# Performance work log

Measured on AMD Instinct MI355X. Metric: run time of the kernel, lower is better.

## Reference

```python
import jax, jax.numpy as jnp
import numpy as np

N, E, G = 100000, 1600000, 1000
F_IN, H, C = 16, 64, 2
EPS = 1e-5


def setup_inputs() -> dict:
    key = jax.random.key(0)
    ks = jax.random.split(key, 8)

    def lin(k, i, o):
        return (jax.random.normal(k, (i, o), jnp.float32) / np.float32(np.sqrt(i)))

    return {
        "x": jax.random.normal(ks[0], (N, F_IN), jnp.float32),
        "edge_index": jax.random.randint(ks[1], (2, E), 0, N),
        "batch": jnp.sort(jax.random.randint(ks[2], (N,), 0, G)),
        # GraphNorm params: weight=1, bias=0, mean_scale(alpha)=1 (PyG init)
        "gn0_w": jnp.ones(F_IN, jnp.float32), "gn0_b": jnp.zeros(F_IN, jnp.float32), "gn0_a": jnp.ones(F_IN, jnp.float32),
        "W1": lin(ks[3], F_IN, H), "b1": jnp.zeros(H, jnp.float32),
        "gn1_w": jnp.ones(H, jnp.float32), "gn1_b": jnp.zeros(H, jnp.float32), "gn1_a": jnp.ones(H, jnp.float32),
        "W2": lin(ks[4], H, H), "b2": jnp.zeros(H, jnp.float32),
        "gn2_w": jnp.ones(H, jnp.float32), "gn2_b": jnp.zeros(H, jnp.float32), "gn2_a": jnp.ones(H, jnp.float32),
        "W3": lin(ks[5], H, H), "b3": jnp.zeros(H, jnp.float32),
        "Wd": lin(ks[6], H, H), "bd": jnp.zeros(H, jnp.float32),
        "Wo": lin(ks[7], H, C), "bo": jnp.zeros(C, jnp.float32),
    }


def _graph_norm(x, batch, w, b, a):
    counts = jnp.maximum(jax.ops.segment_sum(jnp.ones(x.shape[0], x.dtype), batch, G), 1.0)[:, None]
    mean = jax.ops.segment_sum(x, batch, G) / counts          # [G, F]
    out = x - a * mean[batch]
    var = jax.ops.segment_sum(out * out, batch, G) / counts   # [G, F]
    return w * (out * jax.lax.rsqrt(var + EPS)[batch]) + b


def _gcn_conv(x, W, b, src, dst):
    # PyG GCNConv: D^{-1/2}(A+I)D^{-1/2} X W + b, deg includes self-loop
    h = x @ W                                                  # [N, out]
    deg = jax.ops.segment_sum(jnp.ones(src.shape[0], x.dtype), dst, N) + 1.0
    dinv = jax.lax.rsqrt(deg)
    msg = h[src] * (dinv[src] * dinv[dst])[:, None]            # [E, out]
    agg = jax.ops.segment_sum(msg, dst, N) + h / deg[:, None]  # self-loop term: 1/deg
    return agg + b


def reference(x, edge_index, batch, gn0_w, gn0_b, gn0_a, W1, b1,
              gn1_w, gn1_b, gn1_a, W2, b2, gn2_w, gn2_b, gn2_a,
              W3, b3, Wd, bd, Wo, bo):
    src, dst = edge_index[0], edge_index[1]
    x = _graph_norm(x, batch, gn0_w, gn0_b, gn0_a)
    x = jax.nn.relu(_gcn_conv(x, W1, b1, src, dst))
    x = _graph_norm(x, batch, gn1_w, gn1_b, gn1_a)
    x = jax.nn.relu(_gcn_conv(x, W2, b2, src, dst))
    x = _graph_norm(x, batch, gn2_w, gn2_b, gn2_a)
    x = jax.nn.relu(_gcn_conv(x, W3, b3, src, dst))
    counts = jnp.maximum(jax.ops.segment_sum(jnp.ones(N, x.dtype), batch, G), 1.0)
    pooled = jax.ops.segment_sum(x, batch, G) / counts[:, None]  # global_mean_pool [G, H]
    # dropout p=0.5 is identity in eval mode
    h = jax.nn.relu(pooled @ Wd + bd)
    logits = h @ Wo + bo
    return jax.nn.softmax(logits, axis=1)
```

## Files before the change

### kernel.cpp

```cpp
#include <hip/hip_runtime.h>
#include <hip/hip_fp16.h>
#include <math.h>

#define NB_NODES 100000
#define NB_EDGES 1600000
#define NB_GRAPHS 1000
#define CAP 232
#define NBLK1 400
#define CHUNK 4000
#define NBUCK 391
#define BCAP 4608
constexpr float GN_EPS = 1e-5f;

__global__ __launch_bounds__(256) void k1_hist(const int* __restrict__ dst,
    int* __restrict__ hist, const int* __restrict__ batch, int* __restrict__ gstart) {
    __shared__ int h[NBUCK];
    int tid = threadIdx.x;
    for (int i = tid; i < NBUCK; i += 256) h[i] = 0;
    if (blockIdx.x < 4) {
        int g = blockIdx.x * 256 + tid;
        if (g <= NB_GRAPHS) {
            int lo = 0, hi = NB_NODES;
            while (lo < hi) {
                int mid = (lo + hi) >> 1;
                if (batch[mid] < g) lo = mid + 1; else hi = mid;
            }
            gstart[g] = lo;
        }
    }
    __syncthreads();
    int base = blockIdx.x * CHUNK;
    for (int i = tid; i < CHUNK; i += 256) atomicAdd(&h[dst[base + i] >> 8], 1);
    __syncthreads();
    for (int i = tid; i < NBUCK; i += 256) hist[blockIdx.x * NBUCK + i] = h[i];
}

__global__ __launch_bounds__(512) void k2a_scan(int* __restrict__ hist,
                                                int* __restrict__ total) {
    __shared__ int s[512];
    int b = blockIdx.x;
    int tid = threadIdx.x;
    int v = (tid < NBLK1) ? hist[tid * NBUCK + b] : 0;
    s[tid] = v;
    __syncthreads();
    for (int o = 1; o < 512; o <<= 1) {
        int t = (tid >= o) ? s[tid - o] : 0;
        __syncthreads();
        s[tid] += t;
        __syncthreads();
    }
    if (tid < NBLK1) hist[tid * NBUCK + b] = s[tid] - v;
    if (tid == 511) total[b] = s[511];
}

__global__ __launch_bounds__(256) void k3_scatter(const int* __restrict__ ei,
    const int* __restrict__ hist, const int* __restrict__ total,
    unsigned int* __restrict__ ebuf) {
    __shared__ int cur[NBUCK];
    __shared__ int sc[256];
    int tid = threadIdx.x;
    int e0 = 2 * tid, e1 = 2 * tid + 1;
    int v0 = (e0 < NBUCK) ? total[e0] : 0;
    int v1 = (e1 < NBUCK) ? total[e1] : 0;
    int own = v0 + v1;
    sc[tid] = own;
    __syncthreads();
    for (int o = 1; o < 256; o <<= 1) {
        int t = (tid >= o) ? sc[tid - o] : 0;
        __syncthreads();
        sc[tid] += t;
        __syncthreads();
    }
    int pre = sc[tid] - own;
    if (e0 < NBUCK) cur[e0] = pre + hist[blockIdx.x * NBUCK + e0];
    if (e1 < NBUCK) cur[e1] = pre + v0 + hist[blockIdx.x * NBUCK + e1];
    __syncthreads();
    int eb = blockIdx.x * CHUNK;
    for (int i = tid; i < CHUNK; i += 256) {
        int e = eb + i;
        int sidx = ei[e];
        int d = ei[NB_EDGES + e];
        int pos = atomicAdd(&cur[d >> 8], 1);
        ebuf[pos] = (unsigned int)sidx | ((unsigned int)(d & 255) << 24);
    }
}

__global__ __launch_bounds__(256) void k4_fine(const unsigned int* __restrict__ ebuf,
    const int* __restrict__ total, int* __restrict__ csr_src, int* __restrict__ rowptr,
    float* __restrict__ dinv) {
    __shared__ int arena[2 * BCAP + 768];
    unsigned int* epk = (unsigned int*)arena;
    int* outb  = arena + BCAP;
    int* cnt   = arena + 2 * BCAP;
    int* sbuf  = arena + 2 * BCAP + 256;
    int* cur2  = arena + 2 * BCAP + 512;
    int* bases = arena + 2 * BCAP;
    int b = blockIdx.x;
    int tid = threadIdx.x;
    int e0 = 2 * tid, e1 = 2 * tid + 1;
    int v0 = (e0 < NBUCK) ? total[e0] : 0;
    int v1 = (e1 < NBUCK) ? total[e1] : 0;
    int own = v0 + v1;
    cur2[tid] = own;
    __syncthreads();
    for (int o = 1; o < 256; o <<= 1) {
        int t = (tid >= o) ? cur2[tid - o] : 0;
        __syncthreads();
        cur2[tid] += t;
        __syncthreads();
    }
    int pre = cur2[tid] - own;
    if (e0 < NBUCK) bases[e0] = pre;
    if (e1 < NBUCK) bases[e1] = pre + v0;
    if (tid == 0) bases[NBUCK] = NB_EDGES;
    __syncthreads();
    int eb = bases[b], ee = bases[b + 1];
    __syncthreads();
    int m = ee - eb;
    if (m > BCAP) m = BCAP;
    for (int i = tid; i < m; i += 256) epk[i] = ebuf[eb + i];
    cnt[tid] = 0;
    __syncthreads();
    for (int i = tid; i < m; i += 256) atomicAdd(&cnt[epk[i] >> 24], 1);
    __syncthreads();
    int c = cnt[tid];
    sbuf[tid] = c;
    __syncthreads();
    for (int o = 1; o < 256; o <<= 1) {
        int t = (tid >= o) ? sbuf[tid - o] : 0;
        __syncthreads();
        sbuf[tid] += t;
        __syncthreads();
    }
    int off = sbuf[tid] - c;
    cur2[tid] = off;
    __syncthreads();
    for (int i = tid; i < m; i += 256) {
        unsigned int p = epk[i];
        int r = atomicAdd(&cur2[p >> 24], 1);
        outb[r] = (int)(p & 0x00FFFFFFu);
    }
    __syncthreads();
    for (int i = tid; i < m; i += 256) csr_src[eb + i] = outb[i];
    int node = b * 256 + tid;
    if (node < NB_NODES) {
        rowptr[node] = eb + off;
        dinv[node] = rsqrtf((float)(c + 1));
    }
    if (b == 0 && tid == 0) rowptr[NB_NODES] = NB_EDGES;
}

union HU {
    uint4 u;
    __half2 h[4];
};

__device__ __forceinline__ void pkacc(__half2* a, uint4 v) {
    HU x; x.u = v;
    a[0] = __hadd2(a[0], x.h[0]);
    a[1] = __hadd2(a[1], x.h[1]);
    a[2] = __hadd2(a[2], x.h[2]);
    a[3] = __hadd2(a[3], x.h[3]);
}

__device__ __forceinline__ __half2 shxor_h2(__half2 v, int m) {
    union { __half2 h; int i; } u;
    u.h = v;
    u.i = __shfl_xor(u.i, m, 64);
    return u.h;
}

__device__ __forceinline__ int agg4_core(const uint4* __restrict__ hsv,
    const int* __restrict__ rowptr, const int* __restrict__ csr_src,
    const float* __restrict__ dinv, const float* __restrict__ bias,
    int n0, int e, int lane, int f8, int e8, float r[8]) {
    int i2 = n0 + 2 < e ? n0 + 2 : e;
    int i3 = n0 + 3 < e ? n0 + 3 : e;
    int i4 = n0 + 4 < e ? n0 + 4 : e;
    int r0 = rowptr[n0], r1 = rowptr[n0 + 1], r2 = rowptr[i2];
    int r3 = rowptr[i3], r4 = rowptr[i4];
    int d0 = r1 - r0, d1 = r2 - r1, d2 = r3 - r2, d3 = r4 - r3;
    const uint4 Z = {0u, 0u, 0u, 0u};
    int idx0 = (lane < d0) ? csr_src[r0 + lane] : -1;
    int idx1 = (lane < d1) ? csr_src[r1 + lane] : -1;
    int idx2 = (lane < d2) ? csr_src[r2 + lane] : -1;
    int idx3 = (lane < d3) ? csr_src[r3 + lane] : -1;
    uint4 self = Z;
    if (e8 < 4 && n0 + e8 < e) self = hsv[(size_t)(n0 + e8) * 8 + f8];
    uint4 gA[8];
#pragma unroll
    for (int b = 0; b < 4; b++) {
        int u = __shfl(idx0, b * 8 + e8, 64);
        gA[b] = Z;
        if (u >= 0) gA[b] = hsv[(size_t)u * 8 + f8];
        int v = __shfl(idx1, b * 8 + e8, 64);
        gA[4 + b] = Z;
        if (v >= 0) gA[4 + b] = hsv[(size_t)v * 8 + f8];
    }
    uint4 gB[8];
#pragma unroll
    for (int b = 0; b < 4; b++) {
        int u = __shfl(idx2, b * 8 + e8, 64);
        gB[b] = Z;
        if (u >= 0) gB[b] = hsv[(size_t)u * 8 + f8];
        int v = __shfl(idx3, b * 8 + e8, 64);
        gB[4 + b] = Z;
        if (v >= 0) gB[4 + b] = hsv[(size_t)v * 8 + f8];
    }
    __half2 acc0[4], acc1[4], acc2[4], acc3[4];
    __half2 z2{__half(0.f), __half(0.f)};
    acc0[0] = acc0[1] = acc0[2] = acc0[3] = z2;
    acc1[0] = acc1[1] = acc1[2] = acc1[3] = z2;
    acc2[0] = acc2[1] = acc2[2] = acc2[3] = z2;
    acc3[0] = acc3[1] = acc3[2] = acc3[3] = z2;
    if (e8 == 0) pkacc(acc0, self);
    if (e8 == 1) pkacc(acc1, self);
    if (e8 == 2) pkacc(acc2, self);
    if (e8 == 3) pkacc(acc3, self);
#pragma unroll
    for (int b = 0; b < 4; b++) { pkacc(acc0, gA[b]); pkacc(acc1, gA[4 + b]); }
#pragma unroll
    for (int b = 0; b < 4; b++) { pkacc(acc2, gB[b]); pkacc(acc3, gB[4 + b]); }
    int tb0 = (d0 + 7) >> 3, tb1 = (d1 + 7) >> 3;
    int tb2 = (d2 + 7) >> 3, tb3 = (d3 + 7) >> 3;
    for (int b = 4; b < tb0 && b < 8; b++) {
        int u = __shfl(idx0, b * 8 + e8, 64);
        if (u >= 0) pkacc(acc0, hsv[(size_t)u * 8 + f8]);
    }
    for (int b = 4; b < tb1 && b < 8; b++) {
        int u = __shfl(idx1, b * 8 + e8, 64);
        if (u >= 0) pkacc(acc1, hsv[(size_t)u * 8 + f8]);
    }
    for (int b = 4; b < tb2 && b < 8; b++) {
        int u = __shfl(idx2, b * 8 + e8, 64);
        if (u >= 0) pkacc(acc2, hsv[(size_t)u * 8 + f8]);
    }
    for (int b = 4; b < tb3 && b < 8; b++) {
        int u = __shfl(idx3, b * 8 + e8, 64);
        if (u >= 0) pkacc(acc3, hsv[(size_t)u * 8 + f8]);
    }
    for (int b = 8; b < tb0; b++) {
        int j = r0 + b * 8 + e8;
        if (j < r1) pkacc(acc0, hsv[(size_t)csr_src[j] * 8 + f8]);
    }
    for (int b = 8; b < tb1; b++) {
        int j = r1 + b * 8 + e8;
        if (j < r2) pkacc(acc1, hsv[(size_t)csr_src[j] * 8 + f8]);
    }
    for (int b = 8; b < tb2; b++) {
        int j = r2 + b * 8 + e8;
        if (j < r3) pkacc(acc2, hsv[(size_t)csr_src[j] * 8 + f8]);
    }
    for (int b = 8; b < tb3; b++) {
        int j = r3 + b * 8 + e8;
        if (j < r4) pkacc(acc3, hsv[(size_t)csr_src[j] * 8 + f8]);
    }
#pragma unroll
    for (int c = 0; c < 4; c++) {
        __half2 t0 = acc0[c];
        t0 = __hadd2(t0, shxor_h2(t0, 8));
        t0 = __hadd2(t0, shxor_h2(t0, 16));
        t0 = __hadd2(t0, shxor_h2(t0, 32));
        acc0[c] = t0;
        __half2 t1 = acc1[c];
        t1 = __hadd2(t1, shxor_h2(t1, 8));
        t1 = __hadd2(t1, shxor_h2(t1, 16));
        t1 = __hadd2(t1, shxor_h2(t1, 32));
        acc1[c] = t1;
        __half2 t2 = acc2[c];
        t2 = __hadd2(t2, shxor_h2(t2, 8));
        t2 = __hadd2(t2, shxor_h2(t2, 16));
        t2 = __hadd2(t2, shxor_h2(t2, 32));
        acc2[c] = t2;
        __half2 t3 = acc3[c];
        t3 = __hadd2(t3, shxor_h2(t3, 8));
        t3 = __hadd2(t3, shxor_h2(t3, 16));
        t3 = __hadd2(t3, shxor_h2(t3, 32));
        acc3[c] = t3;
    }
    if (e8 >= 4) return -1;
    int node = n0 + e8;
    if (node >= e) return -1;
    const __half2* acc = (e8 == 0) ? acc0 : (e8 == 1) ? acc1 : (e8 == 2) ? acc2 : acc3;
    float dn = dinv[node];
    const float4* b4 = (const float4*)bias;
    float4 blo = b4[f8 * 2], bhi = b4[f8 * 2 + 1];
    float2 f0 = __half22float2(acc[0]);
    float2 f1 = __half22float2(acc[1]);
    float2 f2 = __half22float2(acc[2]);
    float2 f3 = __half22float2(acc[3]);
    r[0] = fmaf(f0.x, dn, blo.x); r[1] = fmaf(f0.y, dn, blo.y);
    r[2] = fmaf(f1.x, dn, blo.z); r[3] = fmaf(f1.y, dn, blo.w);
    r[4] = fmaf(f2.x, dn, bhi.x); r[5] = fmaf(f2.y, dn, bhi.y);
    r[6] = fmaf(f2.x, dn, bhi.z); r[6] = fmaf(f3.x, dn, bhi.z); r[7] = fmaf(f3.y, dn, bhi.w);
#pragma unroll
    for (int c = 0; c < 8; c++) r[c] = r[c] > 0.f ? r[c] : 0.f;
    return node;
}

__device__ __forceinline__ void aggnorm_body(__half* rows, int s, int cnt, int e,
    const uint4* __restrict__ hsv, const int* __restrict__ rowptr,
    const int* __restrict__ csr_src, const float* __restrict__ dinv,
    const float* __restrict__ bias, const float* __restrict__ gw,
    const float* __restrict__ gb, const float* __restrict__ ga,
    const float* __restrict__ W, __half* __restrict__ out,
    float* red, float* red2, float* sam, float* ssc, float* srow) {
    int tid = threadIdx.x, lane = tid & 63, wid = tid >> 6;
    int f8 = lane & 7, e8 = lane >> 3;
    int passes = (cnt + 15) >> 4;
    for (int p = 0; p < passes; ++p) {
        int n0 = __builtin_amdgcn_readfirstlane(s + p * 16 + wid * 4);
        if (n0 < e) {
            float r[8];
            int node = agg4_core(hsv, rowptr, csr_src, dinv, bias, n0, e, lane, f8, e8, r);
            if (node >= 0) {
                HU o;
                o.h[0] = __floats2half2_rn(r[0], r[1]);
                o.h[1] = __floats2half2_rn(r[2], r[3]);
                o.h[2] = __floats2half2_rn(r[4], r[5]);
                o.h[3] = __floats2half2_rn(r[6], r[7]);
                ((uint4*)rows)[(size_t)(node - s) * 8 + f8] = o.u;
            }
        }
    }
    __syncthreads();
    float cntf = (float)(cnt > 1 ? cnt : 1);
    float sum = 0.f, sq = 0.f;
    for (int i = wid; i < cnt; i += 4) {
        float v = __half2float(rows[(size_t)i * 64 + lane]);
        sum += v;
        sq = fmaf(v, v, sq);
    }
    red[tid] = sum; red2[tid] = sq;
    __syncthreads();
    for (int st = 2; st > 0; st >>= 1) {
        if (wid < st) { red[tid] += red[tid + st * 64]; red2[tid] += red2[tid + st * 64]; }
        __syncthreads();
    }
    if (tid < 64) {
        float m = red[tid] / cntf, q = red2[tid] / cntf;
        float am = ga[tid] * m;
        sam[tid] = am;
        ssc[tid] = gw[tid] * rsqrtf(q - 2.f * am * m + am * am + GN_EPS);
    }
    __syncthreads();
    float wcol[64];
#pragma unroll
    for (int k = 0; k < 64; k++) wcol[k] = W[k * 64 + lane];
    float am = sam[lane], sc = ssc[lane], bb = gb[lane];
    for (int i = wid; i < cnt; i += 4) {
        float nv = (__half2float(rows[(size_t)i * 64 + lane]) - am) * sc + bb;
        srow[wid * 64 + lane] = nv;
        float acc = 0.f;
#pragma unroll
        for (int k = 0; k < 64; k++) acc = fmaf(srow[wid * 64 + k], wcol[k], acc);
        out[(size_t)(s + i) * 64 + lane] = __float2half(acc * dinv[s + i]);
    }
}

__global__ __launch_bounds__(256, 4) void fused_aggnorm_k(
    const __half* __restrict__ hs_in, const int* __restrict__ gstart,
    const int* __restrict__ rowptr, const int* __restrict__ csr_src,
    const float* __restrict__ dinv, const float* __restrict__ bias,
    const float* __restrict__ gw, const float* __restrict__ gb,
    const float* __restrict__ ga, const float* __restrict__ W,
    __half* __restrict__ out, __half* __restrict__ spill) {
    __shared__ alignas(16) __half sA[CAP * 64];
    __shared__ float red[256], red2[256];
    __shared__ float sam[64], ssc[64];
    __shared__ float srow[4 * 64];
    int g = blockIdx.x;
    int s = gstart[g], e = gstart[g + 1], cnt = e - s;
    const uint4* hsv = (const uint4*)hs_in;
    if (cnt <= CAP)
        aggnorm_body(sA, s, cnt, e, hsv, rowptr, csr_src, dinv, bias,
                     gw, gb, ga, W, out, red, red2, sam, ssc, srow);
    else
        aggnorm_body(spill + (size_t)s * 64, s, cnt, e, hsv, rowptr, csr_src, dinv, bias,
                     gw, gb, ga, W, out, red, red2, sam, ssc, srow);
}

__global__ __launch_bounds__(256, 4) void fused_aggpool_k(
    const __half* __restrict__ hs_in, const int* __restrict__ gstart,
    const int* __restrict__ rowptr, const int* __restrict__ csr_src,
    const float* __restrict__ dinv, const float* __restrict__ bias,
    const float* __restrict__ Wd, const float* __restrict__ bd,
    const float* __restrict__ Wo, const float* __restrict__ bo,
    float* __restrict__ out) {
    __shared__ float wpart[4 * 64];
    __shared__ float sp[64];
    __shared__ float sh[64];
    __shared__ float sl[2];
    int tid = threadIdx.x, lane = tid & 63, wid = tid >> 6;
    int f8 = lane & 7, e8 = lane >> 3;
    int g = blockIdx.x;
    int s = gstart[g], e = gstart[g + 1], cnt = e - s;
    const uint4* hsv = (const uint4*)hs_in;
    float pacc[8];
#pragma unroll
    for (int j = 0; j < 8; j++) pacc[j] = 0.f;
    int passes = (cnt + 15) >> 4;
    for (int p = 0; p < passes; ++p) {
        int n0 = __builtin_amdgcn_readfirstlane(s + p * 16 + wid * 4);
        if (n0 < e) {
            float r[8];
            int node = agg4_core(hsv, rowptr, csr_src, dinv, bias, n0, e, lane, f8, e8, r);
            if (node >= 0) {
#pragma unroll
                for (int j = 0; j < 8; j++) pacc[j] += r[j];
            }
        }
    }
#pragma unroll
    for (int j = 0; j < 8; j++) {
        float v = pacc[j];
        v += __shfl_xor(v, 8, 64);
        v += __shfl_xor(v, 16, 64);
        v += __shfl_xor(v, 32, 64);
        pacc[j] = v;
    }
    if (lane < 8) {
#pragma unroll
        for (int j = 0; j < 8; j++) wpart[wid * 64 + lane * 8 + j] = pacc[j];
    }
    __syncthreads();
    float cntf = (float)(cnt > 1 ? cnt : 1);
    if (tid < 64)
        sp[tid] = (wpart[tid] + wpart[64 + tid] + wpart[128 + tid] + wpart[192 + tid]) / cntf;
    __syncthreads();
    if (tid < 64) {
        float acc = bd[tid];
        for (int k = 0; k < 64; k++) acc = fmaf(sp[k], Wd[k * 64 + tid], acc);
        sh[tid] = acc > 0.f ? acc : 0.f;
    }
    __syncthreads();
    if (tid < 2) {
        float l = bo[tid];
        for (int k = 0; k < 64; k++) l = fmaf(sh[k], Wo[k * 2 + tid], l);
        sl[tid] = l;
    }
    __syncthreads();
    if (tid < 2) {
        float m = fmaxf(sl[0], sl[1]);
        float e0 = expf(sl[0] - m), e1 = expf(sl[1] - m);
        out[g * 2 + tid] = (tid == 0 ? e0 : e1) / (e0 + e1);
    }
}

__device__ __forceinline__ void l0_body(float* rows, int cnt, int s,
    const float* __restrict__ x, const float* __restrict__ gw,
    const float* __restrict__ gb, const float* __restrict__ ga,
    const float* sW, const float* __restrict__ dinv, __half* __restrict__ hs_out,
    float* red, float* red2, float* sstat, float* sscale, int tid) {
    int f = tid & 15, r = tid >> 4;
    int lane = tid & 63, wid = tid >> 6;
    float cntf = (float)(cnt > 1 ? cnt : 1);
    float sum = 0.f, sq = 0.f;
    for (int i = r; i < cnt; i += 32) {
        float v = x[(size_t)(s + i) * 16 + f];
        rows[i * 16 + f] = v;
        sum += v;
        sq = fmaf(v, v, sq);
    }
    red[tid] = sum; red2[tid] = sq;
    __syncthreads();
    for (int st = 16; st > 0; st >>= 1) {
        if (r < st) { red[tid] += red[tid + st * 16]; red2[tid] += red2[tid + st * 16]; }
        __syncthreads();
    }
    if (tid < 16) {
        float m = red[tid] / cntf, q = red2[tid] / cntf;
        float am = ga[tid] * m;
        sstat[tid] = am;
        sscale[tid] = gw[tid] * rsqrtf(q - 2.f * am * m + am * am + GN_EPS);
    }
    __syncthreads();
    float am = sstat[f], sc = sscale[f], bb = gb[f];
    for (int i = r; i < cnt; i += 32) rows[i * 16 + f] = (rows[i * 16 + f] - am) * sc + bb;
    __syncthreads();
    for (int i = wid; i < cnt; i += 8) {
        float acc = 0.f;
#pragma unroll
        for (int k = 0; k < 16; k++) acc = fmaf(rows[i * 16 + k], sW[k * 64 + lane], acc);
        hs_out[(size_t)(s + i) * 64 + lane] = __float2half(acc * dinv[s + i]);
    }
}

__global__ __launch_bounds__(512) void layer0_k(const float* __restrict__ x,
    const int* __restrict__ gstart, const float* __restrict__ gw,
    const float* __restrict__ gb, const float* __restrict__ ga,
    const float* __restrict__ W, const float* __restrict__ dinv,
    __half* __restrict__ hs_out, float* __restrict__ spill16) {
    __shared__ float sRows[CAP * 16];
    __shared__ float sW[16 * 64];
    __shared__ float red[512], red2[512];
    __shared__ float sstat[16], sscale[16];
    int tid = threadIdx.x;
    int g = blockIdx.x;
    int s = gstart[g], e = gstart[g + 1], cnt = e - s;
    for (int i = tid; i < 16 * 64; i += 512) sW[i] = W[i];
    __syncthreads();
    if (cnt <= CAP)
        l0_body(sRows, cnt, s, x, gw, gb, ga, sW, dinv, hs_out, red, red2, sstat, sscale, tid);
    else
        l0_body(spill16 + (size_t)s * 16, cnt, s, x, gw, gb, ga, sW, dinv, hs_out, red, red2, sstat, sscale, tid);
}

extern "C" void kernel_launch(void* const* d_in, const int* in_sizes, int n_in,
                              void* d_out, int out_size, void* d_ws, size_t ws_size,
                              hipStream_t stream) {
    const float* x    = (const float*)d_in[0];
    const int* ei     = (const int*)d_in[1];
    const int* batch  = (const int*)d_in[2];
    const float* gn0w = (const float*)d_in[3];
    const float* gn0b = (const float*)d_in[4];
    const float* gn0a = (const float*)d_in[5];
    const float* W1   = (const float*)d_in[6];
    const float* b1   = (const float*)d_in[7];
    const float* gn1w = (const float*)d_in[8];
    const float* gn1b = (const float*)d_in[9];
    const float* gn1a = (const float*)d_in[10];
    const float* W2   = (const float*)d_in[11];
    const float* b2   = (const float*)d_in[12];
    const float* gn2w = (const float*)d_in[13];
    const float* gn2b = (const float*)d_in[14];
    const float* gn2a = (const float*)d_in[15];
    const float* W3   = (const float*)d_in[16];
    const float* b3   = (const float*)d_in[17];
    const float* Wd   = (const float*)d_in[18];
    const float* bd   = (const float*)d_in[19];
    const float* Wo   = (const float*)d_in[20];
    const float* bo   = (const float*)d_in[21];

    char* p = (char*)d_ws;
    auto alloc = [&](size_t bytes) -> void* {
        void* r = (void*)p;
        p += (bytes + 255) & ~(size_t)255;
        return r;
    };
    __half* A        = (__half*)alloc((size_t)NB_NODES * 64 * 2);
    __half* B        = (__half*)alloc((size_t)NB_NODES * 64 * 2);
    int* rowptr      = (int*)alloc((size_t)(NB_NODES + 1) * 4);
    unsigned* ebuf   = (unsigned*)alloc((size_t)NB_EDGES * 4);
    int* csr_src     = (int*)alloc((size_t)NB_EDGES * 4);
    int* hist        = (int*)alloc((size_t)NBLK1 * NBUCK * 4);
    int* total       = (int*)alloc((size_t)NBUCK * 4);
    float* dinv      = (float*)alloc((size_t)NB_NODES * 4);
    int* gstart      = (int*)alloc((size_t)(NB_GRAPHS + 1) * 4);
    float* spill16   = (float*)alloc((size_t)NB_NODES * 16 * 4);
    __half* spillH   = (__half*)alloc((size_t)NB_NODES * 64 * 2);

    k1_hist<<<NBLK1, 256, 0, stream>>>(ei + NB_EDGES, hist, batch, gstart);
    k2a_scan<<<NBUCK, 512, 0, stream>>>(hist, total);
    k3_scatter<<<NBLK1, 256, 0, stream>>>(ei, hist, total, ebuf);
    k4_fine<<<NBUCK, 256, 0, stream>>>(ebuf, total, csr_src, rowptr, dinv);

    layer0_k<<<NB_GRAPHS, 512, 0, stream>>>(x, gstart, gn0w, gn0b, gn0a, W1, dinv, B, spill16);
    fused_aggnorm_k<<<NB_GRAPHS, 256, 0, stream>>>(B, gstart, rowptr, csr_src, dinv,
                                                   b1, gn1w, gn1b, gn1a, W2, A, spillH);
    fused_aggnorm_k<<<NB_GRAPHS, 256, 0, stream>>>(A, gstart, rowptr, csr_src, dinv,
                                                   b2, gn2w, gn2b, gn2a, W3, B, spillH);
    fused_aggpool_k<<<NB_GRAPHS, 256, 0, stream>>>(B, gstart, rowptr, csr_src, dinv,
                                                   b3, Wd, bd, Wo, bo, (float*)d_out);
}
```

Measured before the change: 299.8 us.

## Aggregate layer-1 on 16-wide normalized features before applying W1

Layer 0 now stores the normalized, dinv-scaled 16-feature input in fp16 instead of the 64-wide X·W1 product. A new fused layer-1 kernel gathers neighbor rows at 16 features and only then multiplies by W1, using the identity A(XW)=(AX)W. This cuts gather traffic for the first aggregation by four times. CAP is lowered so that shared memory fits the extra buffers, which sends more graphs to the global spill path. The change also fixes a duplicated assignment in the bias/relu helper.

Measured after the change: 296.5 us. No clear change (-1.1%).

```diff
diff --git a/kernel.cpp b/kernel.cpp
--- a/kernel.cpp
+++ b/kernel.cpp
@@ -5,7 +5,7 @@
 #define NB_NODES 100000
 #define NB_EDGES 1600000
 #define NB_GRAPHS 1000
-#define CAP 232
+#define CAP 160
 #define NBLK1 400
 #define CHUNK 4000
 #define NBUCK 391
@@ -292,7 +292,7 @@
     r[0] = fmaf(f0.x, dn, blo.x); r[1] = fmaf(f0.y, dn, blo.y);
     r[2] = fmaf(f1.x, dn, blo.z); r[3] = fmaf(f1.y, dn, blo.w);
     r[4] = fmaf(f2.x, dn, bhi.x); r[5] = fmaf(f2.y, dn, bhi.y);
-    r[6] = fmaf(f2.x, dn, bhi.z); r[6] = fmaf(f3.x, dn, bhi.z); r[7] = fmaf(f3.y, dn, bhi.w);
+    r[6] = fmaf(f3.x, dn, bhi.z); r[7] = fmaf(f3.y, dn, bhi.w);
 #pragma unroll
     for (int c = 0; c < 8; c++) r[c] = r[c] > 0.f ? r[c] : 0.f;
     return node;
@@ -447,13 +447,200 @@
     }
 }
 
+__device__ __forceinline__ void l1_gather(__half* rows16, int s, int cnt, int e,
+    const uint4* __restrict__ yv, const int* __restrict__ rowptr,
+    const int* __restrict__ csr_src, int tid) {
+    int lane = tid & 63, wid = tid >> 6;
+    int es = lane >> 1, f2 = lane & 1;
+    uint4* r16 = (uint4*)rows16;
+    const uint4 Z = {0u, 0u, 0u, 0u};
+    __half2 z2{__half(0.f), __half(0.f)};
+    int passes = (cnt + 15) >> 4;
+    for (int p = 0; p < passes; ++p) {
+        int lnb = p * 16 + wid * 4;
+        int n0 = __builtin_amdgcn_readfirstlane(s + lnb);
+        if (n0 >= e) continue;
+        int i1 = n0 + 1 < e ? n0 + 1 : e;
+        int i2 = n0 + 2 < e ? n0 + 2 : e;
+        int i3 = n0 + 3 < e ? n0 + 3 : e;
+        int i4 = n0 + 4 < e ? n0 + 4 : e;
+        int r0 = rowptr[n0], r1 = rowptr[i1], r2 = rowptr[i2];
+        int r3 = rowptr[i3], r4 = rowptr[i4];
+        int d0 = r1 - r0, d1 = r2 - r1, d2 = r3 - r2, d3 = r4 - r3;
+        int idx0 = (lane < d0) ? csr_src[r0 + lane] : -1;
+        int idx1 = (lane < d1) ? csr_src[r1 + lane] : -1;
+        int idx2 = (lane < d2) ? csr_src[r2 + lane] : -1;
+        int idx3 = (lane < d3) ? csr_src[r3 + lane] : -1;
+        uint4 self = Z;
+        if (lane < 8 && lnb + (lane >> 1) < cnt)
+            self = yv[(size_t)(s + lnb + (lane >> 1)) * 2 + f2];
+        __half2 a0[4], a1[4], a2[4], a3[4];
+        a0[0] = a0[1] = a0[2] = a0[3] = z2;
+        a1[0] = a1[1] = a1[2] = a1[3] = z2;
+        a2[0] = a2[1] = a2[2] = a2[3] = z2;
+        a3[0] = a3[1] = a3[2] = a3[3] = z2;
+        { int u = __shfl(idx0, es, 64); if (u >= 0) pkacc(a0, yv[(size_t)u * 2 + f2]); }
+        { int u = __shfl(idx1, es, 64); if (u >= 0) pkacc(a1, yv[(size_t)u * 2 + f2]); }
+        { int u = __shfl(idx2, es, 64); if (u >= 0) pkacc(a2, yv[(size_t)u * 2 + f2]); }
+        { int u = __shfl(idx3, es, 64); if (u >= 0) pkacc(a3, yv[(size_t)u * 2 + f2]); }
+        if (d0 > 32) { int u = __shfl(idx0, 32 + es, 64); if (u >= 0) pkacc(a0, yv[(size_t)u * 2 + f2]); }
+        if (d1 > 32) { int u = __shfl(idx1, 32 + es, 64); if (u >= 0) pkacc(a1, yv[(size_t)u * 2 + f2]); }
+        if (d2 > 32) { int u = __shfl(idx2, 32 + es, 64); if (u >= 0) pkacc(a2, yv[(size_t)u * 2 + f2]); }
+        if (d3 > 32) { int u = __shfl(idx3, 32 + es, 64); if (u >= 0) pkacc(a3, yv[(size_t)u * 2 + f2]); }
+        for (int b = 2; b * 32 < d0; ++b) { int t = b * 32 + es; if (t < d0) pkacc(a0, yv[(size_t)csr_src[r0 + t] * 2 + f2]); }
+        for (int b = 2; b * 32 < d1; ++b) { int t = b * 32 + es; if (t < d1) pkacc(a1, yv[(size_t)csr_src[r1 + t] * 2 + f2]); }
+        for (int b = 2; b * 32 < d2; ++b) { int t = b * 32 + es; if (t < d2) pkacc(a2, yv[(size_t)csr_src[r2 + t] * 2 + f2]); }
+        for (int b = 2; b * 32 < d3; ++b) { int t = b * 32 + es; if (t < d3) pkacc(a3, yv[(size_t)csr_src[r3 + t] * 2 + f2]); }
+#pragma unroll
+        for (int j = 0; j < 4; ++j) {
+            __half2 t;
+            t = a0[j];
+            t = __hadd2(t, shxor_h2(t, 2));
+            t = __hadd2(t, shxor_h2(t, 4));
+            t = __hadd2(t, shxor_h2(t, 8));
+            t = __hadd2(t, shxor_h2(t, 16));
+            t = __hadd2(t, shxor_h2(t, 32));
+            a0[j] = t;
+            t = a1[j];
+            t = __hadd2(t, shxor_h2(t, 2));
+            t = __hadd2(t, shxor_h2(t, 4));
+            t = __hadd2(t, shxor_h2(t, 8));
+            t = __hadd2(t, shxor_h2(t, 16));
+            t = __hadd2(t, shxor_h2(t, 32));
+            a1[j] = t;
+            t = a2[j];
+            t = __hadd2(t, shxor_h2(t, 2));
+            t = __hadd2(t, shxor_h2(t, 4));
+            t = __hadd2(t, shxor_h2(t, 8));
+            t = __hadd2(t, shxor_h2(t, 16));
+            t = __hadd2(t, shxor_h2(t, 32));
+            a2[j] = t;
+            t = a3[j];
+            t = __hadd2(t, shxor_h2(t, 2));
+            t = __hadd2(t, shxor_h2(t, 4));
+            t = __hadd2(t, shxor_h2(t, 8));
+            t = __hadd2(t, shxor_h2(t, 16));
+            t = __hadd2(t, shxor_h2(t, 32));
+            a3[j] = t;
+        }
+        if (lane < 8) {
+            int k = lane >> 1;
+            int ln = lnb + k;
+            if (ln < cnt) {
+                __half2 sel[4];
+#pragma unroll
+                for (int j = 0; j < 4; ++j)
+                    sel[j] = (k == 0) ? a0[j] : (k == 1) ? a1[j] : (k == 2) ? a2[j] : a3[j];
+                pkacc(sel, self);
+                HU o;
+                o.h[0] = sel[0]; o.h[1] = sel[1]; o.h[2] = sel[2]; o.h[3] = sel[3];
+                r16[(size_t)ln * 2 + f2] = o.u;
+            }
+        }
+    }
+}
+
+__device__ __forceinline__ void l1_body(__half* rows64, __half* rows16,
+    int s, int cnt, int e,
+    const uint4* __restrict__ yv, const int* __restrict__ rowptr,
+    const int* __restrict__ csr_src, const float* __restrict__ dinv,
+    const float* __restrict__ W1, const float* __restrict__ b1,
+    const float* __restrict__ gw, const float* __restrict__ gb,
+    const float* __restrict__ ga, const float* __restrict__ W2,
+    __half* __restrict__ out,
+    float* red, float* red2, float* sam, float* ssc, float* srow) {
+    int tid = threadIdx.x, lane = tid & 63, wid = tid >> 6;
+    l1_gather(rows16, s, cnt, e, yv, rowptr, csr_src, tid);
+    __syncthreads();
+    float w1c[16];
+#pragma unroll
+    for (int k = 0; k < 16; ++k) w1c[k] = W1[k * 64 + lane];
+    float bb1 = b1[lane];
+    const uint4* r16v = (const uint4*)rows16;
+    float cntf = (float)(cnt > 1 ? cnt : 1);
+    float sum = 0.f, sq = 0.f;
+    for (int i = wid; i < cnt; i += 4) {
+        HU q0, q1;
+        q0.u = r16v[(size_t)i * 2];
+        q1.u = r16v[(size_t)i * 2 + 1];
+        float dn = dinv[s + i];
+        float dot = 0.f;
+#pragma unroll
+        for (int j = 0; j < 4; ++j) {
+            float2 v = __half22float2(q0.h[j]);
+            dot = fmaf(v.x, w1c[2 * j], dot);
+            dot = fmaf(v.y, w1c[2 * j + 1], dot);
+        }
+#pragma unroll
+        for (int j = 0; j < 4; ++j) {
+            float2 v = __half22float2(q1.h[j]);
+            dot = fmaf(v.x, w1c[8 + 2 * j], dot);
+            dot = fmaf(v.y, w1c[8 + 2 * j + 1], dot);
+        }
+        float h = fmaf(dot, dn, bb1);
+        h = h > 0.f ? h : 0.f;
+        rows64[(size_t)i * 64 + lane] = __float2half(h);
+        sum += h;
+        sq = fmaf(h, h, sq);
+    }
+    red[tid] = sum; red2[tid] = sq;
+    __syncthreads();
+    for (int st = 2; st > 0; st >>= 1) {
+        if (wid < st) { red[tid] += red[tid + st * 64]; red2[tid] += red2[tid + st * 64]; }
+        __syncthreads();
+    }
+    if (tid < 64) {
+        float m = red[tid] / cntf, q = red2[tid] / cntf;
+        float am = ga[tid] * m;
+        sam[tid] = am;
+        ssc[tid] = gw[tid] * rsqrtf(q - 2.f * am * m + am * am + GN_EPS);
+    }
+    __syncthreads();
+    float wcol[64];
+#pragma unroll
+    for (int k = 0; k < 64; k++) wcol[k] = W2[k * 64 + lane];
+    float am = sam[lane], sc = ssc[lane], bbg = gb[lane];
+    for (int i = wid; i < cnt; i += 4) {
+        float nv = (__half2float(rows64[(size_t)i * 64 + lane]) - am) * sc + bbg;
+        srow[wid * 64 + lane] = nv;
+        float acc = 0.f;
+#pragma unroll
+        for (int k = 0; k < 64; k++) acc = fmaf(srow[wid * 64 + k], wcol[k], acc);
+        out[(size_t)(s + i) * 64 + lane] = __float2half(acc * dinv[s + i]);
+    }
+}
+
+__global__ __launch_bounds__(256, 4) void fused_l1_k(
+    const __half* __restrict__ y16, const int* __restrict__ gstart,
+    const int* __restrict__ rowptr, const int* __restrict__ csr_src,
+    const float* __restrict__ dinv, const float* __restrict__ W1,
+    const float* __restrict__ b1, const float* __restrict__ gw,
+    const float* __restrict__ gb, const float* __restrict__ ga,
+    const float* __restrict__ W2, __half* __restrict__ out,
+    __half* __restrict__ spill64, __half* __restrict__ spill16) {
+    __shared__ alignas(16) __half sR64[CAP * 64];
+    __shared__ alignas(16) __half sR16[CAP * 16];
+    __shared__ float red[256], red2[256];
+    __shared__ float sam[64], ssc[64];
+    __shared__ float srow[4 * 64];
+    int g = blockIdx.x;
+    int s = gstart[g], e = gstart[g + 1], cnt = e - s;
+    const uint4* yv = (const uint4*)y16;
+    if (cnt <= CAP)
+        l1_body(sR64, sR16, s, cnt, e, yv, rowptr, csr_src, dinv,
+                W1, b1, gw, gb, ga, W2, out, red, red2, sam, ssc, srow);
+    else
+        l1_body(spill64 + (size_t)s * 64, spill16 + (size_t)s * 16, s, cnt, e,
+                yv, rowptr, csr_src, dinv,
+                W1, b1, gw, gb, ga, W2, out, red, red2, sam, ssc, srow);
+}
+
 __device__ __forceinline__ void l0_body(float* rows, int cnt, int s,
     const float* __restrict__ x, const float* __restrict__ gw,
     const float* __restrict__ gb, const float* __restrict__ ga,
-    const float* sW, const float* __restrict__ dinv, __half* __restrict__ hs_out,
+    const float* __restrict__ dinv, __half* __restrict__ y16,
     float* red, float* red2, float* sstat, float* sscale, int tid) {
     int f = tid & 15, r = tid >> 4;
-    int lane = tid & 63, wid = tid >> 6;
     float cntf = (float)(cnt > 1 ? cnt : 1);
     float sum = 0.f, sq = 0.f;
     for (int i = r; i < cnt; i += 32) {
@@ -476,34 +663,27 @@
     }
     __syncthreads();
     float am = sstat[f], sc = sscale[f], bb = gb[f];
-    for (int i = r; i < cnt; i += 32) rows[i * 16 + f] = (rows[i * 16 + f] - am) * sc + bb;
-    __syncthreads();
-    for (int i = wid; i < cnt; i += 8) {
-        float acc = 0.f;
-#pragma unroll
-        for (int k = 0; k < 16; k++) acc = fmaf(rows[i * 16 + k], sW[k * 64 + lane], acc);
-        hs_out[(size_t)(s + i) * 64 + lane] = __float2half(acc * dinv[s + i]);
+    for (int i = r; i < cnt; i += 32) {
+        float nv = (rows[i * 16 + f] - am) * sc + bb;
+        y16[(size_t)(s + i) * 16 + f] = __float2half(nv * dinv[s + i]);
     }
 }
 
 __global__ __launch_bounds__(512) void layer0_k(const float* __restrict__ x,
     const int* __restrict__ gstart, const float* __restrict__ gw,
     const float* __restrict__ gb, const float* __restrict__ ga,
-    const float* __restrict__ W, const float* __restrict__ dinv,
-    __half* __restrict__ hs_out, float* __restrict__ spill16) {
+    const float* __restrict__ dinv, __half* __restrict__ y16,
+    float* __restrict__ spill16f) {
     __shared__ float sRows[CAP * 16];
-    __shared__ float sW[16 * 64];
     __shared__ float red[512], red2[512];
     __shared__ float sstat[16], sscale[16];
     int tid = threadIdx.x;
     int g = blockIdx.x;
     int s = gstart[g], e = gstart[g + 1], cnt = e - s;
-    for (int i = tid; i < 16 * 64; i += 512) sW[i] = W[i];
-    __syncthreads();
     if (cnt <= CAP)
-        l0_body(sRows, cnt, s, x, gw, gb, ga, sW, dinv, hs_out, red, red2, sstat, sscale, tid);
+        l0_body(sRows, cnt, s, x, gw, gb, ga, dinv, y16, red, red2, sstat, sscale, tid);
     else
-        l0_body(spill16 + (size_t)s * 16, cnt, s, x, gw, gb, ga, sW, dinv, hs_out, red, red2, sstat, sscale, tid);
+        l0_body(spill16f + (size_t)s * 16, cnt, s, x, gw, gb, ga, dinv, y16, red, red2, sstat, sscale, tid);
 }
 
 extern "C" void kernel_launch(void* const* d_in, const int* in_sizes, int n_in,
@@ -540,6 +720,7 @@
     };
     __half* A        = (__half*)alloc((size_t)NB_NODES * 64 * 2);
     __half* B        = (__half*)alloc((size_t)NB_NODES * 64 * 2);
+    __half* y16      = (__half*)alloc((size_t)NB_NODES * 16 * 2);
     int* rowptr      = (int*)alloc((size_t)(NB_NODES + 1) * 4);
     unsigned* ebuf   = (unsigned*)alloc((size_t)NB_EDGES * 4);
     int* csr_src     = (int*)alloc((size_t)NB_EDGES * 4);
@@ -547,17 +728,18 @@
     int* total       = (int*)alloc((size_t)NBUCK * 4);
     float* dinv      = (float*)alloc((size_t)NB_NODES * 4);
     int* gstart      = (int*)alloc((size_t)(NB_GRAPHS + 1) * 4);
-    float* spill16   = (float*)alloc((size_t)NB_NODES * 16 * 4);
+    float* spill16f  = (float*)alloc((size_t)NB_NODES * 16 * 4);
     __half* spillH   = (__half*)alloc((size_t)NB_NODES * 64 * 2);
+    __half* spillQ   = (__half*)alloc((size_t)NB_NODES * 16 * 2);
 
     k1_hist<<<NBLK1, 256, 0, stream>>>(ei + NB_EDGES, hist, batch, gstart);
     k2a_scan<<<NBUCK, 512, 0, stream>>>(hist, total);
     k3_scatter<<<NBLK1, 256, 0, stream>>>(ei, hist, total, ebuf);
     k4_fine<<<NBUCK, 256, 0, stream>>>(ebuf, total, csr_src, rowptr, dinv);
 
-    layer0_k<<<NB_GRAPHS, 512, 0, stream>>>(x, gstart, gn0w, gn0b, gn0a, W1, dinv, B, spill16);
-    fused_aggnorm_k<<<NB_GRAPHS, 256, 0, stream>>>(B, gstart, rowptr, csr_src, dinv,
-                                                   b1, gn1w, gn1b, gn1a, W2, A, spillH);
+    layer0_k<<<NB_GRAPHS, 512, 0, stream>>>(x, gstart, gn0w, gn0b, gn0a, dinv, y16, spill16f);
+    fused_l1_k<<<NB_GRAPHS, 256, 0, stream>>>(y16, gstart, rowptr, csr_src, dinv,
+                                              W1, b1, gn1w, gn1b, gn1a, W2, A, spillH, spillQ);
     fused_aggnorm_k<<<NB_GRAPHS, 256, 0, stream>>>(A, gstart, rowptr, csr_src, dinv,
                                                    b2, gn2w, gn2b, gn2a, W3, B, spillH);
     fused_aggpool_k<<<NB_GRAPHS, 256, 0, stream>>>(B, gstart, rowptr, csr_src, dinv,
```
